# Kernel optimization log

Hardware: AMD Instinct MI355X
Metric: run time of the kernel (lower is better)

## Reference

```python
import jax, jax.numpy as jnp
import numpy as np
from jax import lax
from jax.scipy.special import logsumexp

XY, Z, V, WS = 16, 8, 10000, 2
S = XY * XY * Z            # 2048 states
EMB, TOK, HID = 256, 100, 256
B, T, L = 8, 16, 12
EPS = 1e-5


def residual(x, w1, b1, w2, b2, g, beta):
    # ResidualLayer: relu(lin1) -> relu(lin2) -> LayerNorm(x2 + x1)
    x1 = jax.nn.relu(x @ w1.T + b1)
    x2 = jax.nn.relu(x1 @ w2.T + b2)
    h = x2 + x1
    mu = h.mean(-1, keepdims=True)
    var = ((h - mu) ** 2).mean(-1, keepdims=True)
    return (h - mu) * lax.rsqrt(var + EPS) * g + beta


def win_logmean(m, axis, ws):
    win = 2 * ws + 1
    pads = [(0, 0)] * m.ndim
    pads[axis] = (ws, ws)
    p = jnp.pad(m, pads, mode='edge')
    d = m.shape[axis]
    acc = lax.dynamic_slice_in_dim(p, 0, d, axis)
    for k in range(1, win):
        acc = jnp.logaddexp(acc, lax.dynamic_slice_in_dim(p, k, d, axis))
    return acc - jnp.log(jnp.float32(win))


def setup_inputs() -> dict:
    key = jax.random.key(0)
    it = iter(jax.random.split(key, 64))

    def rn(shape, scale=0.05):
        return jax.random.normal(next(it), shape, jnp.float32) * scale

    inp = {}
    inp['state_emb'] = jax.random.normal(next(it), (S, EMB), jnp.float32)
    inp['tok_emb'] = jax.random.normal(next(it), (V, TOK), jnp.float32)

    def res(pfx, din, dout):
        inp[pfx + '_w1'] = rn((dout, din))
        inp[pfx + '_b1'] = jnp.zeros((dout,), jnp.float32)
        inp[pfx + '_w2'] = rn((dout, dout))
        inp[pfx + '_b2'] = jnp.zeros((dout,), jnp.float32)
        inp[pfx + '_g'] = jnp.ones((dout,), jnp.float32)
        inp[pfx + '_beta'] = jnp.zeros((dout,), jnp.float32)

    res('start', EMB, HID)
    inp['start_wo'] = rn((1, HID))
    inp['start_bo'] = jnp.zeros((1,), jnp.float32)
    res('tin', EMB, HID)
    res('tout', EMB, HID)
    res('emit', EMB, TOK)
    inp['stories'] = jax.random.randint(next(it), (B, T, L), 0, V + 1)  # id V = pad
    inp['story_length'] = T
    return inp


def reference(state_emb, tok_emb,
              start_w1, start_b1, start_w2, start_b2, start_g, start_beta, start_wo, start_bo,
              tin_w1, tin_b1, tin_w2, tin_b2, tin_g, tin_beta,
              tout_w1, tout_b1, tout_w2, tout_b2, tout_g, tout_beta,
              emit_w1, emit_b1, emit_w2, emit_b2, emit_g, emit_beta,
              stories, story_length):
    # prior_log_p: [S]
    h0 = residual(state_emb, start_w1, start_b1, start_w2, start_b2, start_g, start_beta)
    priors = jax.nn.log_softmax((h0 @ start_wo.T + start_bo)[:, 0], axis=-1)

    # transition_log_p: sparse-neighbor masked [S,S] log-softmax
    h_in = residual(state_emb, tin_w1, tin_b1, tin_w2, tin_b2, tin_g, tin_beta)
    h_out = residual(state_emb, tout_w1, tout_b1, tout_w2, tout_b2, tout_g, tout_beta)
    trans = h_in @ h_out.T
    idx = jnp.arange(S)
    offs = jnp.array([0, 1, -1, XY, -XY, XY * XY, 2 * XY * XY])
    neigh = idx[:, None] + offs[None, :]                        # [S,7]
    allowed = (neigh[:, :, None] == idx[None, None, :]).any(1)  # allowed[j,i]
    trans = jax.nn.log_softmax(jnp.where(allowed, trans, -jnp.inf), axis=-1)

    # emission matrix with windowed log-mean pooling over x,y
    h_emit = residual(state_emb, emit_w1, emit_b1, emit_w2, emit_b2, emit_g, emit_beta)
    em = jax.nn.log_softmax(h_emit @ tok_emb.T, axis=1)         # [S,V]
    em = em.reshape(Z, XY, XY, V)
    em = win_logmean(em, 2, WS)   # dim -2
    em = win_logmean(em, 1, WS)   # dim -3
    em = em.reshape(S, V)
    em_pad = jnp.concatenate([em, jnp.zeros((S, 1), em.dtype)], axis=1)  # pad token
    emis = em_pad.T[stories].sum(2)                             # [B,T,S]

    # HMM forward recursion in log domain
    score0 = emis[:, 0] + priors[None, :]

    def step(score, em_t):
        new = em_t + logsumexp(trans[None, :, :] + score[:, None, :], axis=-1)
        return new, new

    _, rest = lax.scan(step, score0, jnp.moveaxis(emis[:, 1:story_length], 1, 0))
    return jnp.concatenate([score0[None], rest], axis=0)        # [T,B,S]
```

## Files before the change

### kernel.cpp

```cpp
#include <hip/hip_runtime.h>
#include <hip/hip_bf16.h>
#include <math.h>


typedef __bf16 bf16_t;
typedef __bf16 bf16x8 __attribute__((ext_vector_type(8)));
typedef float  floatx4 __attribute__((ext_vector_type(4)));
typedef short  short8  __attribute__((ext_vector_type(8)));

#define S_TOT 2048
#define NT2 79
#define LSE_LD 80

struct GJob {
    const float*  Af;
    const bf16_t* Ab;
    int lda;
    const float* B; int ldb;
    int N, Nrows, K, Kvalid;
    float* C; int ldc;
    const float* bias; int nbias;
    const float* addm; int ldadd;
    bf16_t* Cbf; int ldcb;
};
struct GJobs { GJob j[4]; };

#define BM 64
#define BN 64
#define LDT 72

template<int EPI, int A32>
__global__ __launch_bounds__(256) void gemm_k(GJobs jobs) {
    GJob jb = jobs.j[blockIdx.z];
    const int m0 = blockIdx.x * BM;
    const int n0 = blockIdx.y * BN;
    if (n0 >= jb.N) return;

    __shared__ alignas(16) bf16_t As[BM * LDT];
    __shared__ alignas(16) bf16_t Bs[BN * LDT];
    const int tid  = threadIdx.x;
    const int lane = tid & 63, wave = tid >> 6;
    const int wm = (wave & 1) * 32, wn = (wave >> 1) * 32;
    const int sr = tid >> 2, scc = (tid & 3) * 16;
    const int qm = lane & 15, qk = (lane >> 4) * 8;

    floatx4 acc[2][2];
    floatx4 zf = {0.f, 0.f, 0.f, 0.f};
#pragma unroll
    for (int i = 0; i < 2; i++)
#pragma unroll
        for (int j = 0; j < 2; j++) acc[i][j] = zf;

    const bool brv = (n0 + sr) < jb.Nrows;

    for (int k0 = 0; k0 < jb.K; k0 += 64) {
        if constexpr (A32) {
            const float* Ar = jb.Af + (size_t)(m0 + sr) * jb.lda + k0 + scc;
            alignas(16) bf16_t ta[16];
#pragma unroll
            for (int i = 0; i < 4; i++) {
                float4 f = ((const float4*)Ar)[i];
                ta[i * 4 + 0] = (bf16_t)f.x; ta[i * 4 + 1] = (bf16_t)f.y;
                ta[i * 4 + 2] = (bf16_t)f.z; ta[i * 4 + 3] = (bf16_t)f.w;
            }
            *(short8*)&As[sr * LDT + scc]     = *(short8*)&ta[0];
            *(short8*)&As[sr * LDT + scc + 8] = *(short8*)&ta[8];
        } else {
            const bf16_t* Ar = jb.Ab + (size_t)(m0 + sr) * jb.lda + k0 + scc;
            *(short8*)&As[sr * LDT + scc]     = *(const short8*)&Ar[0];
            *(short8*)&As[sr * LDT + scc + 8] = *(const short8*)&Ar[8];
        }
        {
            const float* Br = jb.B + (size_t)(n0 + sr) * jb.ldb + k0 + scc;
            alignas(16) bf16_t tb[16];
#pragma unroll
            for (int i = 0; i < 4; i++) {
                int c4 = k0 + scc + i * 4;
                float4 f = {0.f, 0.f, 0.f, 0.f};
                if (brv && c4 < jb.Kvalid) f = *(const float4*)&Br[i * 4];
                tb[i * 4 + 0] = (bf16_t)f.x; tb[i * 4 + 1] = (bf16_t)f.y;
                tb[i * 4 + 2] = (bf16_t)f.z; tb[i * 4 + 3] = (bf16_t)f.w;
            }
            *(short8*)&Bs[sr * LDT + scc]     = *(short8*)&tb[0];
            *(short8*)&Bs[sr * LDT + scc + 8] = *(short8*)&tb[8];
        }
        __syncthreads();
#pragma unroll
        for (int kk = 0; kk < 2; kk++) {
            int qo = kk * 32 + qk;
            bf16x8 a[2], b[2];
            a[0] = *(const bf16x8*)&As[(wm + qm) * LDT + qo];
            a[1] = *(const bf16x8*)&As[(wm + 16 + qm) * LDT + qo];
            b[0] = *(const bf16x8*)&Bs[(wn + qm) * LDT + qo];
            b[1] = *(const bf16x8*)&Bs[(wn + 16 + qm) * LDT + qo];
#pragma unroll
            for (int mi = 0; mi < 2; mi++)
#pragma unroll
                for (int ni = 0; ni < 2; ni++)
                    acc[mi][ni] = __builtin_amdgcn_mfma_f32_16x16x32_bf16(a[mi], b[ni], acc[mi][ni], 0, 0, 0);
        }
        __syncthreads();
    }

    const int cl = lane & 15, rq = (lane >> 4) * 4;
#pragma unroll
    for (int mi = 0; mi < 2; mi++)
#pragma unroll
        for (int ni = 0; ni < 2; ni++)
#pragma unroll
            for (int r = 0; r < 4; r++) {
                int gm = m0 + wm + mi * 16 + rq + r;
                int gn = n0 + wn + ni * 16 + cl;
                if (gn < jb.N) {
                    float bv = (gn < jb.nbias) ? jb.bias[gn] : 0.f;
                    float v = fmaxf(acc[mi][ni][r] + bv, 0.f);
                    if constexpr (EPI == 1) {
                        jb.C[(size_t)gm * jb.ldc + gn] = v;
                        jb.Cbf[(size_t)gm * jb.ldcb + gn] = (bf16_t)v;
                    } else {
                        jb.C[(size_t)gm * jb.ldc + gn] = v + jb.addm[(size_t)gm * jb.ldadd + gn];
                    }
                }
            }
}

struct LJob {
    const float* h; int ld, dout;
    const float* g; const float* beta;
    float* of32; int ldo;
    bf16_t* obf; int ldob; int padN;
    const float* wo; const float* bo; float* praw;
};
struct LJobs { LJob j[4]; };

__global__ __launch_bounds__(256) void ln_k(LJobs jobs) {
    LJob jb = jobs.j[blockIdx.y];
    __shared__ float red[256];
    int row = blockIdx.x, t = threadIdx.x;
    float hv = (t < jb.dout) ? jb.h[(size_t)row * jb.ld + t] : 0.f;
    red[t] = hv;
    __syncthreads();
#pragma unroll
    for (int s = 128; s > 0; s >>= 1) { if (t < s) red[t] += red[t + s]; __syncthreads(); }
    float mu = red[0] / jb.dout;
    __syncthreads();
    float d = (t < jb.dout) ? (hv - mu) : 0.f;
    red[t] = d * d;
    __syncthreads();
#pragma unroll
    for (int s = 128; s > 0; s >>= 1) { if (t < s) red[t] += red[t + s]; __syncthreads(); }
    float var = red[0] / jb.dout;
    float rstd = rsqrtf(var + 1e-5f);
    float y = 0.f;
    if (t < jb.dout) {
        y = d * rstd * jb.g[t] + jb.beta[t];
        if (jb.of32) jb.of32[(size_t)row * jb.ldo + t] = y;
        if (jb.obf)  jb.obf[(size_t)row * jb.ldob + t] = (bf16_t)y;
    } else if (jb.obf && t < jb.padN) {
        jb.obf[(size_t)row * jb.ldob + t] = (bf16_t)0.f;
    }
    if (jb.wo) {
        __syncthreads();
        red[t] = (t < jb.dout) ? y * jb.wo[t] : 0.f;
        __syncthreads();
#pragma unroll
        for (int s = 128; s > 0; s >>= 1) { if (t < s) red[t] += red[t + s]; __syncthreads(); }
        if (t == 0) jb.praw[row] = red[0] + jb.bo[0];
    }
}

__global__ __launch_bounds__(256) void trans_k(const float* __restrict__ hin,
                                               const float* __restrict__ hout,
                                               float* __restrict__ tr,
                                               const float* __restrict__ praw,
                                               float* __restrict__ plse)
{
    __shared__ float red[256];
    if (blockIdx.x == 512) {
        int t = threadIdx.x;
        float v[8];
        float m = -INFINITY;
#pragma unroll
        for (int i = 0; i < 8; i++) { v[i] = praw[t * 8 + i]; m = fmaxf(m, v[i]); }
        red[t] = m;
        __syncthreads();
#pragma unroll
        for (int s = 128; s > 0; s >>= 1) { if (t < s) red[t] = fmaxf(red[t], red[t + s]); __syncthreads(); }
        float M = red[0];
        __syncthreads();
        float ss = 0.f;
#pragma unroll
        for (int i = 0; i < 8; i++) ss += __expf(v[i] - M);
        red[t] = ss;
        __syncthreads();
#pragma unroll
        for (int s = 128; s > 0; s >>= 1) { if (t < s) red[t] += red[t + s]; __syncthreads(); }
        if (t == 0) plse[0] = M + __logf(red[0]);
        return;
    }
    const int OFFS[7] = {0, 1, -1, 16, -16, 256, 512};
    int j = blockIdx.x * 4 + (threadIdx.x >> 6);
    int lane = threadIdx.x & 63;
    float4 a = ((const float4*)(hin + (size_t)j * 256))[lane];
    float d[7];
#pragma unroll
    for (int k = 0; k < 7; k++) {
        int i = j + OFFS[k];
        float pdot = 0.f;
        if ((unsigned)i < 2048u) {
            float4 b = ((const float4*)(hout + (size_t)i * 256))[lane];
            pdot = a.x * b.x + a.y * b.y + a.z * b.z + a.w * b.w;
        }
#pragma unroll
        for (int o = 32; o > 0; o >>= 1) pdot += __shfl_down(pdot, o);
        d[k] = pdot;
    }
    if (lane == 0) {
        float m = -INFINITY;
#pragma unroll
        for (int k = 0; k < 7; k++) { int i = j + OFFS[k]; if ((unsigned)i < 2048u) m = fmaxf(m, d[k]); }
        float ss = 0.f;
#pragma unroll
        for (int k = 0; k < 7; k++) { int i = j + OFFS[k]; if ((unsigned)i < 2048u) ss += __expf(d[k] - m); }
        float l = __logf(ss);
#pragma unroll
        for (int k = 0; k < 7; k++) {
            int i = j + OFFS[k];
            tr[(size_t)j * 8 + k] = ((unsigned)i < 2048u) ? (d[k] - m - l) : -INFINITY;
        }
        tr[(size_t)j * 8 + 7] = -INFINITY;
    }
}

#define LDT2 72
__global__ __launch_bounds__(256) void lse_gemm_k(
    const bf16_t* __restrict__ hemit, const float* __restrict__ tok_emb,
    float* __restrict__ Pmax, float* __restrict__ Psum)
{
    __shared__ alignas(16) bf16_t As[128 * LDT2];
    __shared__ alignas(16) bf16_t Bs[128 * LDT2];
    __shared__ float pmS[2][128];
    __shared__ float psS[2][128];
    const int mb = blockIdx.x * 128;
    const int n0 = blockIdx.y * 128;
    const int tid  = threadIdx.x;
    const int lane = tid & 63, wave = tid >> 6;
    const int wm = (wave & 1) * 64, wn = (wave >> 1) * 64;
    const int sr2 = tid >> 1, scc2 = (tid & 1) * 32;
    const int qm = lane & 15, qk = (lane >> 4) * 8;

    floatx4 acc[4][4];
    floatx4 zf = {0.f, 0.f, 0.f, 0.f};
#pragma unroll
    for (int i = 0; i < 4; i++)
#pragma unroll
        for (int j = 0; j < 4; j++) acc[i][j] = zf;

    const bool brv = (n0 + sr2) < 10000;
    const float* Brow = tok_emb + (size_t)(n0 + sr2) * 100;
    const bf16_t* Arow = hemit + (size_t)(mb + sr2) * 128;

#pragma unroll
    for (int k0 = 0; k0 < 128; k0 += 64) {
#pragma unroll
        for (int i = 0; i < 4; i++)
            *(short8*)&As[sr2 * LDT2 + scc2 + i * 8] = *(const short8*)&Arow[k0 + scc2 + i * 8];
        {
            alignas(16) bf16_t tb[32];
#pragma unroll
            for (int i = 0; i < 8; i++) {
                int c4 = k0 + scc2 + i * 4;
                float4 f = {0.f, 0.f, 0.f, 0.f};
                if (brv && c4 < 100) f = *(const float4*)&Brow[c4];
                tb[i * 4 + 0] = (bf16_t)f.x; tb[i * 4 + 1] = (bf16_t)f.y;
                tb[i * 4 + 2] = (bf16_t)f.z; tb[i * 4 + 3] = (bf16_t)f.w;
            }
#pragma unroll
            for (int i = 0; i < 4; i++)
                *(short8*)&Bs[sr2 * LDT2 + scc2 + i * 8] = *(short8*)&tb[i * 8];
        }
        __syncthreads();
#pragma unroll
        for (int kk = 0; kk < 2; kk++) {
            int qo = kk * 32 + qk;
            bf16x8 a[4], b[4];
#pragma unroll
            for (int mi = 0; mi < 4; mi++) a[mi] = *(const bf16x8*)&As[(wm + mi * 16 + qm) * LDT2 + qo];
#pragma unroll
            for (int ni = 0; ni < 4; ni++) b[ni] = *(const bf16x8*)&Bs[(wn + ni * 16 + qm) * LDT2 + qo];
#pragma unroll
            for (int mi = 0; mi < 4; mi++)
#pragma unroll
                for (int ni = 0; ni < 4; ni++)
                    acc[mi][ni] = __builtin_amdgcn_mfma_f32_16x16x32_bf16(a[mi], b[ni], acc[mi][ni], 0, 0, 0);
        }
        __syncthreads();
    }

    const int cl = lane & 15, rq = (lane >> 4) * 4;
    const int half = wn >> 6;
#pragma unroll
    for (int mi = 0; mi < 4; mi++) {
#pragma unroll
        for (int r = 0; r < 4; r++) {
            float mm = -INFINITY;
#pragma unroll
            for (int ni = 0; ni < 4; ni++) {
                int gcol = n0 + wn + ni * 16 + cl;
                if (gcol < 10000) mm = fmaxf(mm, acc[mi][ni][r]);
            }
            mm = fmaxf(mm, __shfl_xor(mm, 1));
            mm = fmaxf(mm, __shfl_xor(mm, 2));
            mm = fmaxf(mm, __shfl_xor(mm, 4));
            mm = fmaxf(mm, __shfl_xor(mm, 8));
            float ss = 0.f;
#pragma unroll
            for (int ni = 0; ni < 4; ni++) {
                int gcol = n0 + wn + ni * 16 + cl;
                if (gcol < 10000) ss += __expf(acc[mi][ni][r] - mm);
            }
            ss += __shfl_xor(ss, 1);
            ss += __shfl_xor(ss, 2);
            ss += __shfl_xor(ss, 4);
            ss += __shfl_xor(ss, 8);
            if (cl == 0) {
                int row = wm + mi * 16 + rq + r;
                pmS[half][row] = mm;
                psS[half][row] = ss;
            }
        }
    }
    __syncthreads();
    if (tid < 128) {
        float ma = pmS[0][tid], mb2 = pmS[1][tid];
        float M = fmaxf(ma, mb2);
        float S = psS[0][tid] * __expf(ma - M) + psS[1][tid] * __expf(mb2 - M);
        Pmax[(size_t)(mb + tid) * LSE_LD + blockIdx.y] = M;
        Psum[(size_t)(mb + tid) * LSE_LD + blockIdx.y] = S;
    }
}

__global__ __launch_bounds__(256) void lse_fin_k(const float* __restrict__ Pmax,
                                                 const float* __restrict__ Psum,
                                                 float* __restrict__ lse)
{
    int s = (blockIdx.x * 256 + threadIdx.x) >> 6;
    int lane = threadIdx.x & 63;
    const float* pm = Pmax + (size_t)s * LSE_LD;
    const float* ps = Psum + (size_t)s * LSE_LD;
    float pv[2], sv[2];
    float m = -INFINITY;
#pragma unroll
    for (int i = 0; i < 2; i++) {
        int nb = i * 64 + lane;
        bool ok = nb < NT2;
        pv[i] = ok ? pm[nb] : -INFINITY;
        sv[i] = ok ? ps[nb] : 0.f;
        m = fmaxf(m, pv[i]);
    }
#pragma unroll
    for (int o = 1; o < 64; o <<= 1) m = fmaxf(m, __shfl_xor(m, o));
    float ss = 0.f;
#pragma unroll
    for (int i = 0; i < 2; i++) if (sv[i] > 0.f) ss += sv[i] * __expf(pv[i] - m);
#pragma unroll
    for (int o = 1; o < 64; o <<= 1) ss += __shfl_xor(ss, o);
    if (lane == 0) lse[s] = m + __logf(ss);
}

#define ELDT 136
__global__ __launch_bounds__(256) void empool_k(
    const float* __restrict__ tok_emb, const int* __restrict__ stories,
    const bf16_t* __restrict__ hemit, const float* __restrict__ lse,
    float* __restrict__ emis)
{
    __shared__ alignas(16) bf16_t As[16 * ELDT];
    __shared__ float Cs[16][260];
    __shared__ float sm2[256];
    __shared__ int stok[12];
    const int bt = blockIdx.x, z = blockIdx.y, t = threadIdx.x;
    if (t < 12) stok[t] = stories[bt * 12 + t];
    __syncthreads();
    {
        int row = t >> 4, c0 = (t & 15) * 8;
        int tok = (row < 12) ? stok[row] : 10000;
        const float* src = tok_emb + (size_t)tok * 100;
#pragma unroll
        for (int c = 0; c < 8; c++) {
            int cc = c0 + c;
            float v = (tok < 10000 && cc < 100) ? src[cc] : 0.f;
            As[row * ELDT + cc] = (bf16_t)v;
        }
    }
    __syncthreads();

    const int lane = t & 63, wave = t >> 6;
    const int qm = lane & 15, q = lane >> 4;
    floatx4 acc[4];
    floatx4 zf = {0.f, 0.f, 0.f, 0.f};
#pragma unroll
    for (int j = 0; j < 4; j++) acc[j] = zf;

#pragma unroll
    for (int kk = 0; kk < 4; kk++) {
        bf16x8 a = *(const bf16x8*)&As[qm * ELDT + kk * 32 + q * 8];
#pragma unroll
        for (int j = 0; j < 4; j++) {
            int nrow = z * 256 + (wave * 4 + j) * 16 + qm;
            bf16x8 b = *(const bf16x8*)&hemit[(size_t)nrow * 128 + kk * 32 + q * 8];
            acc[j] = __builtin_amdgcn_mfma_f32_16x16x32_bf16(a, b, acc[j], 0, 0, 0);
        }
    }
    {
        const int cl = lane & 15, rq = (lane >> 4) * 4;
#pragma unroll
        for (int j = 0; j < 4; j++) {
            int n = (wave * 4 + j) * 16 + cl;
            float ls = lse[z * 256 + n];
#pragma unroll
            for (int r = 0; r < 4; r++)
                Cs[rq + r][n] = acc[j][r] - ls;
        }
    }
    __syncthreads();

    const int a = t >> 4, b = t & 15;
    float accum = 0.f;
    for (int l = 0; l < 12; l++) {
        float m = -INFINITY;
#pragma unroll
        for (int d = -2; d <= 2; d++) {
            int bb = b + d; bb = bb < 0 ? 0 : (bb > 15 ? 15 : bb);
            m = fmaxf(m, Cs[l][a * 16 + bb]);
        }
        float ss = 0.f;
#pragma unroll
        for (int d = -2; d <= 2; d++) {
            int bb = b + d; bb = bb < 0 ? 0 : (bb > 15 ? 15 : bb);
            ss += __expf(Cs[l][a * 16 + bb] - m);
        }
        sm2[t] = m + __logf(ss);
        __syncthreads();
        float m2 = -INFINITY;
#pragma unroll
        for (int d = -2; d <= 2; d++) {
            int aa = a + d; aa = aa < 0 ? 0 : (aa > 15 ? 15 : aa);
            m2 = fmaxf(m2, sm2[aa * 16 + b]);
        }
        float s2 = 0.f;
#pragma unroll
        for (int d = -2; d <= 2; d++) {
            int aa = a + d; aa = aa < 0 ? 0 : (aa > 15 ? 15 : aa);
            s2 += __expf(sm2[aa * 16 + b] - m2);
        }
        if (stok[l] < 10000) accum += m2 + __logf(s2) - 3.2188758248682006f;
        __syncthreads();
    }
    emis[(size_t)bt * S_TOT + (size_t)z * 256 + t] = accum;
}

__global__ __launch_bounds__(1024) void fwd_k(const float* __restrict__ emm,
                                              const float* __restrict__ praw,
                                              const float* __restrict__ plse,
                                              const float* __restrict__ tr,
                                              float* __restrict__ out)
{
    const int OFFS[7] = {0, 1, -1, 16, -16, 256, 512};
    __shared__ float sc[2][S_TOT];
    int b = blockIdx.x, t = threadIdx.x;
    float pl = plse[0];
    const float* eb = emm + (size_t)b * 16 * S_TOT;

    float e[2][16];
#pragma unroll
    for (int i = 0; i < 2; i++) {
        int j = i * 1024 + t;
#pragma unroll
        for (int tt = 0; tt < 16; tt++) e[i][tt] = eb[tt * S_TOT + j];
    }
    float trj[2][7];
#pragma unroll
    for (int i = 0; i < 2; i++) {
        int j = i * 1024 + t;
        float4 lo = ((const float4*)(tr + (size_t)j * 8))[0];
        float4 hi = ((const float4*)(tr + (size_t)j * 8))[1];
        trj[i][0] = lo.x; trj[i][1] = lo.y; trj[i][2] = lo.z; trj[i][3] = lo.w;
        trj[i][4] = hi.x; trj[i][5] = hi.y; trj[i][6] = hi.z;
    }
#pragma unroll
    for (int i = 0; i < 2; i++) {
        int j = i * 1024 + t;
        float v = e[i][0] + praw[j] - pl;
        sc[0][j] = v;
        out[(size_t)b * S_TOT + j] = v;
    }
    __syncthreads();
#pragma unroll
    for (int tt = 1; tt < 16; tt++) {
        int cur = tt & 1, prv = cur ^ 1;
#pragma unroll
        for (int i = 0; i < 2; i++) {
            int j = i * 1024 + t;
            float x[7];
            float m = -INFINITY;
#pragma unroll
            for (int k = 0; k < 7; k++) {
                int ii = j + OFFS[k];
                ii = ii < 0 ? 0 : (ii > 2047 ? 2047 : ii);
                x[k] = trj[i][k] + sc[prv][ii];
                m = fmaxf(m, x[k]);
            }
            float ss = 0.f;
#pragma unroll
            for (int k = 0; k < 7; k++) ss += __expf(x[k] - m);
            float v = e[i][tt] + m + __logf(ss);
            sc[cur][j] = v;
            out[(size_t)tt * (8 * S_TOT) + (size_t)b * S_TOT + j] = v;
        }
        __syncthreads();
    }
}

extern "C" void kernel_launch(void* const* d_in, const int* in_sizes, int n_in,
                              void* d_out, int out_size, void* d_ws, size_t ws_size,
                              hipStream_t stream)
{
    (void)in_sizes; (void)n_in; (void)out_size; (void)ws_size;
    const float* state_emb  = (const float*)d_in[0];
    const float* tok_emb    = (const float*)d_in[1];
    const float* start_w1   = (const float*)d_in[2];
    const float* start_b1   = (const float*)d_in[3];
    const float* start_w2   = (const float*)d_in[4];
    const float* start_b2   = (const float*)d_in[5];
    const float* start_g    = (const float*)d_in[6];
    const float* start_beta = (const float*)d_in[7];
    const float* start_wo   = (const float*)d_in[8];
    const float* start_bo   = (const float*)d_in[9];
    const float* tin_w1     = (const float*)d_in[10];
    const float* tin_b1     = (const float*)d_in[11];
    const float* tin_w2     = (const float*)d_in[12];
    const float* tin_b2     = (const float*)d_in[13];
    const float* tin_g      = (const float*)d_in[14];
    const float* tin_beta   = (const float*)d_in[15];
    const float* tout_w1    = (const float*)d_in[16];
    const float* tout_b1    = (const float*)d_in[17];
    const float* tout_w2    = (const float*)d_in[18];
    const float* tout_b2    = (const float*)d_in[19];
    const float* tout_g     = (const float*)d_in[20];
    const float* tout_beta  = (const float*)d_in[21];
    const float* emit_w1    = (const float*)d_in[22];
    const float* emit_b1    = (const float*)d_in[23];
    const float* emit_w2    = (const float*)d_in[24];
    const float* emit_b2    = (const float*)d_in[25];
    const float* emit_g     = (const float*)d_in[26];
    const float* emit_beta  = (const float*)d_in[27];
    const int*   stories    = (const int*)d_in[28];
    float* out = (float*)d_out;

    char* base = (char*)d_ws;
    size_t off = 0;
    auto carve = [&](size_t bytes) -> char* {
        char* r = base + off;
        off = (off + bytes + 255) & ~(size_t)255;
        return r;
    };

    bf16_t* hemit = (bf16_t*)carve((size_t)2048 * 128 * 2);
    float*  hin   = (float*)carve((size_t)2048 * 256 * 4);
    float*  hout  = (float*)carve((size_t)2048 * 256 * 4);
    float*  praw  = (float*)carve((size_t)2048 * 4);
    float*  plse  = (float*)carve(256);
    float*  trans = (float*)carve((size_t)2048 * 8 * 4);
    float*  pmax  = (float*)carve((size_t)2048 * LSE_LD * 4);
    float*  psum  = (float*)carve((size_t)2048 * LSE_LD * 4);
    float*  lse   = (float*)carve((size_t)2048 * 4);
    float*  emis  = (float*)carve((size_t)128 * 2048 * 4);

    float*  x1f_s  = (float*)carve((size_t)2048 * 256 * 4);
    float*  x1f_i  = (float*)carve((size_t)2048 * 256 * 4);
    float*  x1f_o  = (float*)carve((size_t)2048 * 256 * 4);
    float*  x1f_e  = (float*)carve((size_t)2048 * 128 * 4);
    bf16_t* x1b_s  = (bf16_t*)carve((size_t)2048 * 256 * 2);
    bf16_t* x1b_i  = (bf16_t*)carve((size_t)2048 * 256 * 2);
    bf16_t* x1b_o  = (bf16_t*)carve((size_t)2048 * 256 * 2);
    bf16_t* x1b_e  = (bf16_t*)carve((size_t)2048 * 128 * 2);
    float*  htmp_s = (float*)carve((size_t)2048 * 256 * 4);
    float*  htmp_i = (float*)carve((size_t)2048 * 256 * 4);
    float*  htmp_o = (float*)carve((size_t)2048 * 256 * 4);
    float*  htmp_e = (float*)carve((size_t)2048 * 128 * 4);

    GJobs g1;
    g1.j[0] = {state_emb, nullptr, 256, start_w1, 256, 256, 256, 256, 256, x1f_s, 256, start_b1, 256, nullptr, 0, x1b_s, 256};
    g1.j[1] = {state_emb, nullptr, 256, tin_w1,   256, 256, 256, 256, 256, x1f_i, 256, tin_b1,   256, nullptr, 0, x1b_i, 256};
    g1.j[2] = {state_emb, nullptr, 256, tout_w1,  256, 256, 256, 256, 256, x1f_o, 256, tout_b1,  256, nullptr, 0, x1b_o, 256};
    g1.j[3] = {state_emb, nullptr, 256, emit_w1,  256, 128, 100, 256, 256, x1f_e, 128, emit_b1,  100, nullptr, 0, x1b_e, 128};
    gemm_k<1, 1><<<dim3(32, 4, 4), 256, 0, stream>>>(g1);

    GJobs g2;
    g2.j[0] = {nullptr, x1b_s, 256, start_w2, 256, 256, 256, 256, 256, htmp_s, 256, start_b2, 256, x1f_s, 256, nullptr, 0};
    g2.j[1] = {nullptr, x1b_i, 256, tin_w2,   256, 256, 256, 256, 256, htmp_i, 256, tin_b2,   256, x1f_i, 256, nullptr, 0};
    g2.j[2] = {nullptr, x1b_o, 256, tout_w2,  256, 256, 256, 256, 256, htmp_o, 256, tout_b2,  256, x1f_o, 256, nullptr, 0};
    g2.j[3] = {nullptr, x1b_e, 128, emit_w2,  100, 128, 100, 128, 100, htmp_e, 128, emit_b2,  100, x1f_e, 128, nullptr, 0};
    gemm_k<2, 0><<<dim3(32, 4, 4), 256, 0, stream>>>(g2);

    LJobs lj;
    lj.j[0] = {htmp_s, 256, 256, start_g, start_beta, nullptr, 0, nullptr, 0, 0, start_wo, start_bo, praw};
    lj.j[1] = {htmp_i, 256, 256, tin_g,   tin_beta,   hin, 256, nullptr, 0, 0, nullptr, nullptr, nullptr};
    lj.j[2] = {htmp_o, 256, 256, tout_g,  tout_beta,  hout, 256, nullptr, 0, 0, nullptr, nullptr, nullptr};
    lj.j[3] = {htmp_e, 128, 100, emit_g,  emit_beta,  nullptr, 0, hemit, 128, 128, nullptr, nullptr, nullptr};
    ln_k<<<dim3(2048, 4), 256, 0, stream>>>(lj);

    trans_k<<<513, 256, 0, stream>>>(hin, hout, trans, praw, plse);

    lse_gemm_k<<<dim3(16, NT2), 256, 0, stream>>>(hemit, tok_emb, pmax, psum);
    lse_fin_k<<<512, 256, 0, stream>>>(pmax, psum, lse);

    empool_k<<<dim3(128, 8), 256, 0, stream>>>(tok_emb, stories, hemit, lse, emis);

    fwd_k<<<8, 1024, 0, stream>>>(emis, praw, plse, trans, out);
}
```

Measured before the change: 223.6 us.

## Pre-convert token embeddings to padded bf16 and load MFMA operands directly

Adds a kernel that converts tok_emb to a zero-padded bf16 [10112x128] buffer once per call. The LSE GEMM then drops its LDS staging and loads MFMA fragments straight from global memory, with no __syncthreads and no fp32-to-bf16 conversion inside the kernel. This removes the repeated conversion across the 16 M-blocks and the shared-memory round trip. In exchange it adds an extra launch and about 2.6MB of write traffic, and the uncoalesced per-lane 16-byte global loads rely on L2 reuse.

```diff
diff --git a/kernel.cpp b/kernel.cpp
--- a/kernel.cpp
+++ b/kernel.cpp
@@ -11,6 +11,15 @@
 #define S_TOT 2048
 #define NT2 79
 #define LSE_LD 80
+#define VPAD 10112
+
+__global__ __launch_bounds__(256) void tokconv_k(const float* __restrict__ src,
+                                                 bf16_t* __restrict__ dst) {
+    int idx = blockIdx.x * 256 + threadIdx.x;
+    int r = idx >> 7, c = idx & 127;
+    float v = (r < 10000 && c < 100) ? src[r * 100 + c] : 0.f;
+    dst[idx] = (bf16_t)v;
+}
 
 struct GJob {
     const float*  Af;
@@ -232,13 +241,10 @@
     }
 }
 
-#define LDT2 72
 __global__ __launch_bounds__(256) void lse_gemm_k(
-    const bf16_t* __restrict__ hemit, const float* __restrict__ tok_emb,
+    const bf16_t* __restrict__ hemit, const bf16_t* __restrict__ tok_bf,
     float* __restrict__ Pmax, float* __restrict__ Psum)
 {
-    __shared__ alignas(16) bf16_t As[128 * LDT2];
-    __shared__ alignas(16) bf16_t Bs[128 * LDT2];
     __shared__ float pmS[2][128];
     __shared__ float psS[2][128];
     const int mb = blockIdx.x * 128;
@@ -246,8 +252,7 @@
     const int tid  = threadIdx.x;
     const int lane = tid & 63, wave = tid >> 6;
     const int wm = (wave & 1) * 64, wn = (wave >> 1) * 64;
-    const int sr2 = tid >> 1, scc2 = (tid & 1) * 32;
-    const int qm = lane & 15, qk = (lane >> 4) * 8;
+    const int qm = lane & 15, q = lane >> 4;
 
     floatx4 acc[4][4];
     floatx4 zf = {0.f, 0.f, 0.f, 0.f};
@@ -256,45 +261,21 @@
 #pragma unroll
         for (int j = 0; j < 4; j++) acc[i][j] = zf;
 
-    const bool brv = (n0 + sr2) < 10000;
-    const float* Brow = tok_emb + (size_t)(n0 + sr2) * 100;
-    const bf16_t* Arow = hemit + (size_t)(mb + sr2) * 128;
-
-#pragma unroll
-    for (int k0 = 0; k0 < 128; k0 += 64) {
-#pragma unroll
-        for (int i = 0; i < 4; i++)
-            *(short8*)&As[sr2 * LDT2 + scc2 + i * 8] = *(const short8*)&Arow[k0 + scc2 + i * 8];
-        {
-            alignas(16) bf16_t tb[32];
-#pragma unroll
-            for (int i = 0; i < 8; i++) {
-                int c4 = k0 + scc2 + i * 4;
-                float4 f = {0.f, 0.f, 0.f, 0.f};
-                if (brv && c4 < 100) f = *(const float4*)&Brow[c4];
-                tb[i * 4 + 0] = (bf16_t)f.x; tb[i * 4 + 1] = (bf16_t)f.y;
-                tb[i * 4 + 2] = (bf16_t)f.z; tb[i * 4 + 3] = (bf16_t)f.w;
-            }
-#pragma unroll
-            for (int i = 0; i < 4; i++)
-                *(short8*)&Bs[sr2 * LDT2 + scc2 + i * 8] = *(short8*)&tb[i * 8];
-        }
-        __syncthreads();
-#pragma unroll
-        for (int kk = 0; kk < 2; kk++) {
-            int qo = kk * 32 + qk;
-            bf16x8 a[4], b[4];
-#pragma unroll
-            for (int mi = 0; mi < 4; mi++) a[mi] = *(const bf16x8*)&As[(wm + mi * 16 + qm) * LDT2 + qo];
-#pragma unroll
-            for (int ni = 0; ni < 4; ni++) b[ni] = *(const bf16x8*)&Bs[(wn + ni * 16 + qm) * LDT2 + qo];
-#pragma unroll
-            for (int mi = 0; mi < 4; mi++)
-#pragma unroll
-                for (int ni = 0; ni < 4; ni++)
-                    acc[mi][ni] = __builtin_amdgcn_mfma_f32_16x16x32_bf16(a[mi], b[ni], acc[mi][ni], 0, 0, 0);
-        }
-        __syncthreads();
+    const bf16_t* Aw = hemit  + (size_t)(mb + wm + qm) * 128 + q * 8;
+    const bf16_t* Bw = tok_bf + (size_t)(n0 + wn + qm) * 128 + q * 8;
+
+#pragma unroll
+    for (int kk = 0; kk < 4; kk++) {
+        bf16x8 a[4], b[4];
+#pragma unroll
+        for (int i = 0; i < 4; i++) a[i] = *(const bf16x8*)&Aw[(size_t)(i * 16) * 128 + kk * 32];
+#pragma unroll
+        for (int i = 0; i < 4; i++) b[i] = *(const bf16x8*)&Bw[(size_t)(i * 16) * 128 + kk * 32];
+#pragma unroll
+        for (int mi = 0; mi < 4; mi++)
+#pragma unroll
+            for (int ni = 0; ni < 4; ni++)
+                acc[mi][ni] = __builtin_amdgcn_mfma_f32_16x16x32_bf16(a[mi], b[ni], acc[mi][ni], 0, 0, 0);
     }
 
     const int cl = lane & 15, rq = (lane >> 4) * 4;
@@ -565,16 +546,17 @@
         return r;
     };
 
-    bf16_t* hemit = (bf16_t*)carve((size_t)2048 * 128 * 2);
-    float*  hin   = (float*)carve((size_t)2048 * 256 * 4);
-    float*  hout  = (float*)carve((size_t)2048 * 256 * 4);
-    float*  praw  = (float*)carve((size_t)2048 * 4);
-    float*  plse  = (float*)carve(256);
-    float*  trans = (float*)carve((size_t)2048 * 8 * 4);
-    float*  pmax  = (float*)carve((size_t)2048 * LSE_LD * 4);
-    float*  psum  = (float*)carve((size_t)2048 * LSE_LD * 4);
-    float*  lse   = (float*)carve((size_t)2048 * 4);
-    float*  emis  = (float*)carve((size_t)128 * 2048 * 4);
+    bf16_t* hemit  = (bf16_t*)carve((size_t)2048 * 128 * 2);
+    bf16_t* tok_bf = (bf16_t*)carve((size_t)VPAD * 128 * 2);
+    float*  hin    = (float*)carve((size_t)2048 * 256 * 4);
+    float*  hout   = (float*)carve((size_t)2048 * 256 * 4);
+    float*  praw   = (float*)carve((size_t)2048 * 4);
+    float*  plse   = (float*)carve(256);
+    float*  trans  = (float*)carve((size_t)2048 * 8 * 4);
+    float*  pmax   = (float*)carve((size_t)2048 * LSE_LD * 4);
+    float*  psum   = (float*)carve((size_t)2048 * LSE_LD * 4);
+    float*  lse    = (float*)carve((size_t)2048 * 4);
+    float*  emis   = (float*)carve((size_t)128 * 2048 * 4);
 
     float*  x1f_s  = (float*)carve((size_t)2048 * 256 * 4);
     float*  x1f_i  = (float*)carve((size_t)2048 * 256 * 4);
@@ -589,6 +571,8 @@
     float*  htmp_o = (float*)carve((size_t)2048 * 256 * 4);
     float*  htmp_e = (float*)carve((size_t)2048 * 128 * 4);
 
+    tokconv_k<<<(VPAD * 128) / 256, 256, 0, stream>>>(tok_emb, tok_bf);
+
     GJobs g1;
     g1.j[0] = {state_emb, nullptr, 256, start_w1, 256, 256, 256, 256, 256, x1f_s, 256, start_b1, 256, nullptr, 0, x1b_s, 256};
     g1.j[1] = {state_emb, nullptr, 256, tin_w1,   256, 256, 256, 256, 256, x1f_i, 256, tin_b1,   256, nullptr, 0, x1b_i, 256};
@@ -612,7 +596,7 @@
 
     trans_k<<<513, 256, 0, stream>>>(hin, hout, trans, praw, plse);
 
-    lse_gemm_k<<<dim3(16, NT2), 256, 0, stream>>>(hemit, tok_emb, pmax, psum);
+    lse_gemm_k<<<dim3(16, NT2), 256, 0, stream>>>(hemit, tok_bf, pmax, psum);
     lse_fin_k<<<512, 256, 0, stream>>>(pmax, psum, lse);
 
     empool_k<<<dim3(128, 8), 256, 0, stream>>>(tok_emb, stories, hemit, lse, emis);
```

Result: no change. 220.3 us, median of 2 (-1.5%).
